# Kernel optimization log

Hardware: AMD Instinct MI355X
Metric: run time of the kernel (lower is better)

Reference implementation:

```python
import jax, jax.numpy as jnp
import numpy as np

B, H, W = 16, 56, 56
CE, CB = 128, 256
NH, WS = 8, 7
HD = CB // NH
N = WS * WS
HID = 4 * CB
EPS = 1e-5


def _rel_pos_index(ws):
    coords = np.stack(np.meshgrid(np.arange(ws), np.arange(ws), indexing='ij')).reshape(2, -1)
    rel = (coords[:, :, None] - coords[:, None, :]).transpose(1, 2, 0).astype(np.int64)
    rel[..., 0] += ws - 1
    rel[..., 1] += ws - 1
    rel[..., 0] *= 2 * ws - 1
    return rel.sum(-1)  # (ws*ws, ws*ws)

RPI = jnp.asarray(_rel_pos_index(WS))


def _ln(x, w, b, axes):
    m = x.mean(axes, keepdims=True)
    v = x.var(axes, keepdims=True)
    return (x - m) * jax.lax.rsqrt(v + EPS) * w + b


def _window_partition(x):  # (B,H,W,C) -> (B*nW, N, C)
    Bx, Hx, Wx, C = x.shape
    x = x.reshape(Bx, Hx // WS, WS, Wx // WS, WS, C)
    return x.transpose(0, 1, 3, 2, 4, 5).reshape(-1, N, C)


def _window_reverse(xw, C):  # (B*nW, N, C) -> (B,H,W,C)
    x = xw.reshape(B, H // WS, W // WS, WS, WS, C)
    return x.transpose(0, 1, 3, 2, 4, 5).reshape(B, H, W, C)


def setup_inputs() -> dict:
    key = jax.random.key(0)
    ks = jax.random.split(key, 12)
    s = 0.02
    return {
        'x_edge': jax.random.normal(ks[0], (B, CE, H, W), jnp.float32),
        'x_body': jax.random.normal(ks[1], (B, H * W, CB), jnp.float32),
        'norm_edge_w': jnp.ones((CE, H, W), jnp.float32),
        'norm_edge_b': jnp.zeros((CE, H, W), jnp.float32),
        'conv_w': jax.random.normal(ks[2], (CB, CE), jnp.float32) * s,
        'norm1_w': jnp.ones((CB,), jnp.float32),
        'norm1_b': jnp.zeros((CB,), jnp.float32),
        'rpb_table': jax.random.normal(ks[3], ((2 * WS - 1) ** 2, NH), jnp.float32) * s,
        'q_w': jax.random.normal(ks[4], (CB, CB), jnp.float32) * s,
        'kv_w': jax.random.normal(ks[5], (2 * CB, CB), jnp.float32) * s,
        'proj_w': jax.random.normal(ks[6], (CB, CB), jnp.float32) * s,
        'proj_b': jnp.zeros((CB,), jnp.float32),
        'norm2_w': jnp.ones((CB,), jnp.float32),
        'norm2_b': jnp.zeros((CB,), jnp.float32),
        'fc1_w': jax.random.normal(ks[7], (HID, CB), jnp.float32) * s,
        'fc1_b': jnp.zeros((HID,), jnp.float32),
        'fc2_w': jax.random.normal(ks[8], (CB, HID), jnp.float32) * s,
        'fc2_b': jnp.zeros((CB,), jnp.float32),
    }


def reference(x_edge, x_body, norm_edge_w, norm_edge_b, conv_w, norm1_w, norm1_b,
              rpb_table, q_w, kv_w, proj_w, proj_b, norm2_w, norm2_b,
              fc1_w, fc1_b, fc2_w, fc2_b):
    x_body_cache = x_body
    scale = HD ** -0.5

    # LayerNorm over (C,H,W) of x_edge, then 1x1 conv (channel mixing), to NHWC
    xe = _ln(x_edge, norm_edge_w, norm_edge_b, axes=(1, 2, 3))  # (B,CE,H,W)
    xe = jnp.einsum('oc,bchw->bhwo', conv_w, xe)                # (B,H,W,CB)

    xb = _ln(x_body, norm1_w, norm1_b, axes=(-1,)).reshape(B, H, W, CB)

    xe_w = _window_partition(xe)  # (Bn,N,CB)
    xb_w = _window_partition(xb)

    q = (xe_w @ q_w.T).reshape(-1, N, NH, HD).transpose(0, 2, 1, 3) * scale  # (Bn,NH,N,HD)
    kv = (xb_w @ kv_w.T).reshape(-1, N, 2, NH, HD).transpose(2, 0, 3, 1, 4)
    k, v = kv[0], kv[1]  # (Bn,NH,N,HD)

    attn = jnp.einsum('bhnd,bhmd->bhnm', q, k)
    bias = rpb_table[RPI.reshape(-1)].reshape(N, N, NH).transpose(2, 0, 1)  # (NH,N,N)
    attn = jax.nn.softmax(attn + bias[None], axis=-1)

    out = jnp.einsum('bhnm,bhmd->bhnd', attn, v).transpose(0, 2, 1, 3).reshape(-1, N, CB)
    out = out @ proj_w.T + proj_b

    x_attn = _window_reverse(out, CB).reshape(B, H * W, CB)
    x = x_body_cache + x_attn

    h = _ln(x, norm2_w, norm2_b, axes=(-1,))
    h = jax.nn.gelu(h @ fc1_w.T + fc1_b, approximate=False) @ fc2_w.T + fc2_b
    x = x + h

    return x.reshape(B, H, W, CB).transpose(0, 3, 1, 2)  # (B,CB,H,W)
```

## Files before the change

### kernel.cpp

```cpp
#include <hip/hip_runtime.h>
#include <hip/hip_bf16.h>
#include <math.h>

#define B_    16
#define CE_   128
#define CB_   256
#define H_    56
#define W_    56
#define NH_   8
#define WS_   7
#define HD_   32
#define NWIN_ 49
#define HW_   3136
#define M_    50176
#define HID_  1024

typedef short bf16x8 __attribute__((ext_vector_type(8)));
typedef float f32x4  __attribute__((ext_vector_type(4)));

__device__ __forceinline__ float waveRedSum(float v) {
#pragma unroll
  for (int off = 32; off; off >>= 1) v += __shfl_xor(v, off, 64);
  return v;
}

__device__ __forceinline__ void load_lds16(const void* g, void* l) {
  __builtin_amdgcn_global_load_lds((__attribute__((address_space(1))) void*)g,
                                   (__attribute__((address_space(3))) void*)l,
                                   16, 0, 0);
}

__global__ void k_stats1(const float* __restrict__ xe, float* __restrict__ part) {
  int blk = blockIdx.x;
  int b = blk >> 6, s = blk & 63;
  const float4* p = (const float4*)(xe + (size_t)b * 401408 + s * 6272);
  float sm = 0.f, s2 = 0.f;
  for (int i = threadIdx.x; i < 1568; i += 256) {
    float4 v = p[i];
    sm += v.x + v.y + v.z + v.w;
    s2 += v.x * v.x + v.y * v.y + v.z * v.z + v.w * v.w;
  }
  sm = waveRedSum(sm); s2 = waveRedSum(s2);
  __shared__ float aux[8];
  int wave = threadIdx.x >> 6, lane = threadIdx.x & 63;
  if (lane == 0) { aux[wave] = sm; aux[4 + wave] = s2; }
  __syncthreads();
  if (threadIdx.x == 0) {
    part[blk * 2]     = aux[0] + aux[1] + aux[2] + aux[3];
    part[blk * 2 + 1] = aux[4] + aux[5] + aux[6] + aux[7];
  }
}

__global__ void k_stats2(const float* __restrict__ part, float* __restrict__ stats) {
  int b = blockIdx.x, lane = threadIdx.x;
  float sm = part[(b * 64 + lane) * 2];
  float s2 = part[(b * 64 + lane) * 2 + 1];
  sm = waveRedSum(sm); s2 = waveRedSum(s2);
  if (lane == 0) {
    float mean = sm / 401408.0f;
    float var  = s2 / 401408.0f - mean * mean;
    stats[b * 2] = mean;
    stats[b * 2 + 1] = rsqrtf(var + 1e-5f);
  }
}

__global__ void k_cast6(const float* __restrict__ s0, const float* __restrict__ s1,
                        const float* __restrict__ s2, const float* __restrict__ s3,
                        const float* __restrict__ s4, const float* __restrict__ s5,
                        __hip_bfloat16* __restrict__ d) {
  size_t i4 = ((size_t)blockIdx.x * 256 + threadIdx.x) * 4;
  if (i4 >= 819200) return;
  const float* src; size_t off;
  if      (i4 < 32768)  { src = s0; off = 0; }
  else if (i4 < 98304)  { src = s1; off = 32768; }
  else if (i4 < 229376) { src = s2; off = 98304; }
  else if (i4 < 294912) { src = s3; off = 229376; }
  else if (i4 < 557056) { src = s4; off = 294912; }
  else                  { src = s5; off = 557056; }
  float4 v = *(const float4*)(src + (i4 - off));
  union { __hip_bfloat16 h[4]; uint2 u; } pk;
  pk.h[0] = __float2bfloat16(v.x);
  pk.h[1] = __float2bfloat16(v.y);
  pk.h[2] = __float2bfloat16(v.z);
  pk.h[3] = __float2bfloat16(v.w);
  *(uint2*)(d + i4) = pk.u;
}

__global__ void k_wqc(const float* __restrict__ qw, const float* __restrict__ cw,
                      __hip_bfloat16* __restrict__ wqc) {
  int o2 = blockIdx.x, c = threadIdx.x;
  float acc = 0.f;
#pragma unroll 4
  for (int o = 0; o < 256; ++o)
    acc += qw[o2 * 256 + o] * cw[o * 128 + c];
  wqc[o2 * 128 + c] = __float2bfloat16(acc * 0.17677669529663687f);
}

__global__ void k_bias_pre(const float* __restrict__ rpb, float* __restrict__ bp) {
  int blk = blockIdx.x;
  int h = blk >> 4, tile = blk & 15;
  int ti = tile >> 2, tj = tile & 3;
  int lane = threadIdx.x;
  int quad = lane >> 4, lm = lane & 15;
  float4 v;
  float* vp = (float*)&v;
#pragma unroll
  for (int r = 0; r < 4; ++r) {
    int i = ti * 16 + quad * 4 + r;
    int j = tj * 16 + lm;
    float b = -1e30f;
    if (i < 49 && j < 49) {
      int rel = (i / 7 - j / 7 + 6) * 13 + (i % 7 - j % 7 + 6);
      b = rpb[rel * 8 + h];
    }
    vp[r] = b;
  }
  *(float4*)&bp[(size_t)(blk * 64 + lane) * 4] = v;
}

__global__ void k_prep_edge(const float* __restrict__ xe,
                            const float* __restrict__ we,
                            const float* __restrict__ be,
                            const float* __restrict__ stats,
                            __hip_bfloat16* __restrict__ Ae) {
  int wb = blockIdx.x;
  int b = wb >> 6, rem = wb & 63;
  int h0 = (rem >> 3) * 7, w0 = (rem & 7) * 7;
  float mean = stats[b * 2], rstd = stats[b * 2 + 1];
  __shared__ __hip_bfloat16 t[49 * 130];
  for (int idx = threadIdx.x; idx < 128 * 49; idx += 256) {
    int c = idx / 49, p = idx % 49;
    int h = h0 + p / 7, w = w0 + p % 7;
    int off = (c * 56 + h) * 56 + w;
    float v = xe[(size_t)b * 401408 + off];
    t[p * 130 + c] = __float2bfloat16((v - mean) * rstd * we[off] + be[off]);
  }
  __syncthreads();
  __hip_bfloat16* dst = Ae + (size_t)wb * 49 * 128;
  for (int idx = threadIdx.x; idx < 49 * 128; idx += 256) {
    int p = idx >> 7, c = idx & 127;
    dst[idx] = t[p * 130 + c];
  }
}

template <bool PERM>
__global__ void k_ln_rows(const float* __restrict__ x,
                          const float* __restrict__ w,
                          const float* __restrict__ bia,
                          __hip_bfloat16* __restrict__ out) {
  int row = blockIdx.x * 4 + (threadIdx.x >> 6);
  int lane = threadIdx.x & 63;
  float4 xv = *(const float4*)(x + (size_t)row * 256 + lane * 4);
  float s  = xv.x + xv.y + xv.z + xv.w;
  float s2 = xv.x * xv.x + xv.y * xv.y + xv.z * xv.z + xv.w * xv.w;
  s = waveRedSum(s); s2 = waveRedSum(s2);
  float mean = s * (1.0f / 256.0f);
  float var  = s2 * (1.0f / 256.0f) - mean * mean;
  float rstd = rsqrtf(var + 1e-5f);
  int orow = row;
  if (PERM) {
    int b = row / 3136, hw = row % 3136;
    int h = hw / 56, ww = hw % 56;
    orow = (b * 64 + (h / 7) * 8 + (ww / 7)) * 49 + (h % 7) * 7 + (ww % 7);
  }
  float4 wv = *(const float4*)(w + lane * 4);
  float4 bv = *(const float4*)(bia + lane * 4);
  union { __hip_bfloat16 h[4]; uint2 u; } pk;
  pk.h[0] = __float2bfloat16((xv.x - mean) * rstd * wv.x + bv.x);
  pk.h[1] = __float2bfloat16((xv.y - mean) * rstd * wv.y + bv.y);
  pk.h[2] = __float2bfloat16((xv.z - mean) * rstd * wv.z + bv.z);
  pk.h[3] = __float2bfloat16((xv.w - mean) * rstd * wv.w + bv.w);
  *(uint2*)(out + (size_t)orow * 256 + lane * 4) = pk.u;
}

template <int EPI, int NX>
__launch_bounds__(256)
__global__ void gemm_bt(const __hip_bfloat16* __restrict__ A,
                        const __hip_bfloat16* __restrict__ Bw,
                        int M, int N, int K,
                        __hip_bfloat16* __restrict__ outb,
                        float* __restrict__ outf,
                        const float* __restrict__ bias,
                        const float* __restrict__ resid) {
  __shared__ __hip_bfloat16 As[4 * 128 * 8];
  __shared__ __hip_bfloat16 Bs[4 * 128 * 8];
  const int tid  = threadIdx.x;
  const int lane = tid & 63;
  const int wave = tid >> 6;
  const int quad = lane >> 4;
  const int lm   = lane & 15;
  const int wm   = (wave & 1) << 6;
  const int wn   = (wave >> 1) << 6;
  const int lin  = blockIdx.x;
  const int slot = lin >> 3;
  const int band = (lin & 7) * 49 + slot / NX;
  const int n0   = (slot % NX) * 128;
  const int m0   = band * 128;

  const int rh = (wave & 1) * 64;
  const int qw = wave >> 1;
  const __hip_bfloat16* Arow = A  + (size_t)(m0 + rh + lane) * K;
  const __hip_bfloat16* Brow = Bw + (size_t)(n0 + rh + lane) * K;

  f32x4 acc[4][4];
#pragma unroll
  for (int i = 0; i < 4; ++i)
#pragma unroll
    for (int j = 0; j < 4; ++j)
#pragma unroll
      for (int r = 0; r < 4; ++r) acc[i][j][r] = 0.f;

  for (int k0 = 0; k0 < K; k0 += 32) {
#pragma unroll
    for (int p = 0; p < 2; ++p) {
      int q = qw + 2 * p;
      load_lds16(Arow + k0 + q * 8, &As[(q * 128 + rh) * 8]);
      load_lds16(Brow + k0 + q * 8, &Bs[(q * 128 + rh) * 8]);
    }
    __syncthreads();
    bf16x8 af[4], bfr[4];
#pragma unroll
    for (int i = 0; i < 4; ++i)
      af[i] = *(const bf16x8*)&As[(quad * 128 + wm + i * 16 + lm) * 8];
#pragma unroll
    for (int j = 0; j < 4; ++j)
      bfr[j] = *(const bf16x8*)&Bs[(quad * 128 + wn + j * 16 + lm) * 8];
#pragma unroll
    for (int i = 0; i < 4; ++i)
#pragma unroll
      for (int j = 0; j < 4; ++j)
        acc[i][j] = __builtin_amdgcn_mfma_f32_16x16x32_bf16(af[i], bfr[j], acc[i][j], 0, 0, 0);
    __syncthreads();
  }

#pragma unroll
  for (int i = 0; i < 4; ++i) {
#pragma unroll
    for (int r = 0; r < 4; ++r) {
      int gm = m0 + wm + i * 16 + quad * 4 + r;
      size_t rowbase;
      if constexpr (EPI == 2) {
        int wb = gm / 49, nn = gm % 49;
        int b = wb >> 6, rem = wb & 63;
        int h = (rem >> 3) * 7 + nn / 7, w = (rem & 7) * 7 + nn % 7;
        rowbase = (size_t)(b * 3136 + h * 56 + w) * 256;
      } else {
        rowbase = (size_t)gm * N;
      }
#pragma unroll
      for (int j = 0; j < 4; ++j) {
        int gn = n0 + wn + j * 16 + lm;
        float v = acc[i][j][r];
        if constexpr (EPI == 0) {
          outb[rowbase + gn] = __float2bfloat16(v);
        } else if constexpr (EPI == 2) {
          outf[rowbase + gn] = v + bias[gn] + resid[rowbase + gn];
        } else if constexpr (EPI == 3) {
          float x = v + bias[gn];
          float y = 0.7978845608028654f * (x + 0.044715f * x * x * x);
          float e = __expf(2.0f * y);
          float th = 1.0f - 2.0f / (e + 1.0f);
          outb[rowbase + gn] = __float2bfloat16(0.5f * x * (1.0f + th));
        } else {
          outf[rowbase + gn] = v + bias[gn] + resid[rowbase + gn];
        }
      }
    }
  }
}

__launch_bounds__(64)
__global__ void k_attn_mfma(const __hip_bfloat16* __restrict__ qb,
                            const __hip_bfloat16* __restrict__ kvb,
                            const float* __restrict__ bp,
                            __hip_bfloat16* __restrict__ ob) {
  int wb = blockIdx.x >> 3;
  int h  = blockIdx.x & 7;
  __shared__ __align__(16) __hip_bfloat16 lds[7424];
  __hip_bfloat16* Qs = lds;
  __hip_bfloat16* Ks = lds + 2560;
  __hip_bfloat16* Vt = lds + 5120;
  __hip_bfloat16* Ps = lds;
  const int lane = threadIdx.x;
  const int quad = lane >> 4, lm = lane & 15;

  const __hip_bfloat16 zb = __float2bfloat16(0.f);
  for (int i = lane; i < 600; i += 64) { Qs[1960 + i] = zb; Ks[1960 + i] = zb; }
  {
    uint4 z; z.x = z.y = z.z = z.w = 0u;
    for (int i = lane; i < 288; i += 64) ((uint4*)Vt)[i] = z;
  }
  {
    int t = lane >> 2, p = lane & 3;
#pragma unroll
    for (int pass = 0; pass < 4; ++pass, t += 16) {
      if (t < 49) {
        size_t rq = (size_t)(wb * 49 + t);
        uint4 qv = *(const uint4*)(qb + rq * 256 + h * 32 + p * 8);
        *(uint4*)&Qs[t * 40 + p * 8] = qv;
        uint4 kv = *(const uint4*)(kvb + rq * 512 + h * 32 + p * 8);
        *(uint4*)&Ks[t * 40 + p * 8] = kv;
        union { uint4 u; __hip_bfloat16 e[8]; } vv;
        vv.u = *(const uint4*)(kvb + rq * 512 + 256 + h * 32 + p * 8);
#pragma unroll
        for (int i = 0; i < 8; ++i) Vt[(p * 8 + i) * 72 + t] = vv.e[i];
      }
    }
  }
  __builtin_amdgcn_s_waitcnt(0);

  bf16x8 qf[4], kf[4];
#pragma unroll
  for (int i = 0; i < 4; ++i) qf[i] = *(const bf16x8*)&Qs[(i * 16 + lm) * 40 + quad * 8];
#pragma unroll
  for (int j = 0; j < 4; ++j) kf[j] = *(const bf16x8*)&Ks[(j * 16 + lm) * 40 + quad * 8];
  f32x4 s[4][4];
#pragma unroll
  for (int i = 0; i < 4; ++i)
#pragma unroll
    for (int j = 0; j < 4; ++j) {
      f32x4 z4; z4[0] = z4[1] = z4[2] = z4[3] = 0.f;
      s[i][j] = __builtin_amdgcn_mfma_f32_16x16x32_bf16(qf[i], kf[j], z4, 0, 0, 0);
    }
#pragma unroll
  for (int ti = 0; ti < 4; ++ti)
#pragma unroll
    for (int tj = 0; tj < 4; ++tj) {
      f32x4 b = *(const f32x4*)&bp[(size_t)(((h * 4 + ti) * 4 + tj) * 64 + lane) * 4];
      s[ti][tj] += b;
    }
  float mrow[4][4], srow[4][4];
#pragma unroll
  for (int ti = 0; ti < 4; ++ti)
#pragma unroll
    for (int r = 0; r < 4; ++r)
      mrow[ti][r] = fmaxf(fmaxf(s[ti][0][r], s[ti][1][r]), fmaxf(s[ti][2][r], s[ti][3][r]));
#pragma unroll
  for (int mask = 1; mask <= 8; mask <<= 1)
#pragma unroll
    for (int ti = 0; ti < 4; ++ti)
#pragma unroll
      for (int r = 0; r < 4; ++r)
        mrow[ti][r] = fmaxf(mrow[ti][r], __shfl_xor(mrow[ti][r], mask, 64));
#pragma unroll
  for (int ti = 0; ti < 4; ++ti)
#pragma unroll
    for (int tj = 0; tj < 4; ++tj)
#pragma unroll
      for (int r = 0; r < 4; ++r)
        s[ti][tj][r] = __expf(s[ti][tj][r] - mrow[ti][r]);
#pragma unroll
  for (int ti = 0; ti < 4; ++ti)
#pragma unroll
    for (int r = 0; r < 4; ++r)
      srow[ti][r] = s[ti][0][r] + s[ti][1][r] + s[ti][2][r] + s[ti][3][r];
#pragma unroll
  for (int mask = 1; mask <= 8; mask <<= 1)
#pragma unroll
    for (int ti = 0; ti < 4; ++ti)
#pragma unroll
      for (int r = 0; r < 4; ++r)
        srow[ti][r] += __shfl_xor(srow[ti][r], mask, 64);
  float inv[4][4];
#pragma unroll
  for (int ti = 0; ti < 4; ++ti)
#pragma unroll
    for (int r = 0; r < 4; ++r)
      inv[ti][r] = 1.0f / srow[ti][r];

#pragma unroll
  for (int ti = 0; ti < 4; ++ti)
#pragma unroll
    for (int tj = 0; tj < 4; ++tj)
#pragma unroll
      for (int r = 0; r < 4; ++r)
        Ps[(ti * 16 + quad * 4 + r) * 72 + tj * 16 + lm] = __float2bfloat16(s[ti][tj][r]);
  __builtin_amdgcn_s_waitcnt(0);

  f32x4 o[4][2];
#pragma unroll
  for (int mt = 0; mt < 4; ++mt)
#pragma unroll
    for (int nt = 0; nt < 2; ++nt)
#pragma unroll
      for (int r = 0; r < 4; ++r) o[mt][nt][r] = 0.f;
#pragma unroll
  for (int kq = 0; kq < 2; ++kq) {
    bf16x8 pa[4], vb[2];
#pragma unroll
    for (int mt = 0; mt < 4; ++mt)
      pa[mt] = *(const bf16x8*)&Ps[(mt * 16 + lm) * 72 + kq * 32 + quad * 8];
#pragma unroll
    for (int nt = 0; nt < 2; ++nt)
      vb[nt] = *(const bf16x8*)&Vt[(nt * 16 + lm) * 72 + kq * 32 + quad * 8];
#pragma unroll
    for (int mt = 0; mt < 4; ++mt)
#pragma unroll
      for (int nt = 0; nt < 2; ++nt)
        o[mt][nt] = __builtin_amdgcn_mfma_f32_16x16x32_bf16(pa[mt], vb[nt], o[mt][nt], 0, 0, 0);
  }
#pragma unroll
  for (int mt = 0; mt < 4; ++mt)
#pragma unroll
    for (int r = 0; r < 4; ++r) {
      int row = mt * 16 + quad * 4 + r;
      if (row < 49) {
#pragma unroll
        for (int nt = 0; nt < 2; ++nt)
          ob[(size_t)(wb * 49 + row) * 256 + h * 32 + nt * 16 + lm] =
              __float2bfloat16(o[mt][nt][r] * inv[mt][r]);
      }
    }
}

__global__ void k_transpose(const float* __restrict__ y, float* __restrict__ out) {
  __shared__ float t[32][33];
  int bb = blockIdx.z;
  int hw0 = blockIdx.x * 32;
  int o0 = blockIdx.y * 32;
  int tx = threadIdx.x, ty = threadIdx.y;
#pragma unroll
  for (int r = 0; r < 4; ++r)
    t[ty + r * 8][tx] = y[(size_t)(bb * 3136 + hw0 + ty + r * 8) * 256 + o0 + tx];
  __syncthreads();
#pragma unroll
  for (int r = 0; r < 4; ++r)
    out[(size_t)(bb * 256 + o0 + ty + r * 8) * 3136 + hw0 + tx] = t[tx][ty + r * 8];
}

extern "C" void kernel_launch(void* const* d_in, const int* in_sizes, int n_in,
                              void* d_out, int out_size, void* d_ws, size_t ws_size,
                              hipStream_t stream) {
  const float* x_edge = (const float*)d_in[0];
  const float* x_body = (const float*)d_in[1];
  const float* ne_w   = (const float*)d_in[2];
  const float* ne_b   = (const float*)d_in[3];
  const float* conv_w = (const float*)d_in[4];
  const float* n1_w   = (const float*)d_in[5];
  const float* n1_b   = (const float*)d_in[6];
  const float* rpb    = (const float*)d_in[7];
  const float* q_w    = (const float*)d_in[8];
  const float* kv_w   = (const float*)d_in[9];
  const float* proj_w = (const float*)d_in[10];
  const float* proj_b = (const float*)d_in[11];
  const float* n2_w   = (const float*)d_in[12];
  const float* n2_b   = (const float*)d_in[13];
  const float* fc1_w  = (const float*)d_in[14];
  const float* fc1_b  = (const float*)d_in[15];
  const float* fc2_w  = (const float*)d_in[16];
  const float* fc2_b  = (const float*)d_in[17];
  float* out = (float*)d_out;
  (void)in_sizes; (void)n_in; (void)out_size; (void)ws_size;

  const size_t SZ_Ae    = (size_t)M_ * 128 * 2;
  const size_t SZ_bf256 = (size_t)M_ * 256 * 2;
  const size_t SZ_bf512 = (size_t)M_ * 512 * 2;
  const size_t SZ_h1    = (size_t)M_ * 1024 * 2;

  char* ws = (char*)d_ws;
  __hip_bfloat16* Wb  = (__hip_bfloat16*)ws;
  float* part  = (float*)(ws + 1638400);
  float* stats = (float*)(ws + 1638400 + 8192);
  float* biasp = (float*)(ws + 1638400 + 8192 + 256);
  __hip_bfloat16* wqc = (__hip_bfloat16*)(ws + 1638400 + 8192 + 256 + 131072);
  char*  P     = ws + 1638400 + 8192 + 256 + 131072 + 65536;
  __hip_bfloat16* w_kv   = Wb + 98304;
  __hip_bfloat16* w_proj = Wb + 229376;
  __hip_bfloat16* w_fc1  = Wb + 294912;
  __hip_bfloat16* w_fc2  = Wb + 557056;
  __hip_bfloat16* Ae    = (__hip_bfloat16*)(P);
  __hip_bfloat16* xbn   = (__hip_bfloat16*)(P + SZ_Ae);
  __hip_bfloat16* qb    = (__hip_bfloat16*)(P + SZ_Ae + SZ_bf256);
  __hip_bfloat16* kvb   = (__hip_bfloat16*)(P + SZ_Ae + 2 * SZ_bf256);
  __hip_bfloat16* attnb = (__hip_bfloat16*)(P + SZ_Ae + 2 * SZ_bf256 + SZ_bf512);
  __hip_bfloat16* h1 = (__hip_bfloat16*)(P);
  char* tail         = P + ((SZ_h1 + 1024 * 1024) & ~(size_t)1023);
  __hip_bfloat16* xn = (__hip_bfloat16*)tail;
  float*          yb = (float*)tail;
  float*          xf = (float*)d_out;

  k_cast6<<<800, 256, 0, stream>>>(conv_w, q_w, kv_w, proj_w, fc1_w, fc2_w, Wb);
  k_wqc<<<256, 128, 0, stream>>>(q_w, conv_w, wqc);
  k_bias_pre<<<128, 64, 0, stream>>>(rpb, biasp);
  k_stats1<<<1024, 256, 0, stream>>>(x_edge, part);
  k_stats2<<<16, 64, 0, stream>>>(part, stats);
  k_prep_edge<<<1024, 256, 0, stream>>>(x_edge, ne_w, ne_b, stats, Ae);
  k_ln_rows<true><<<M_ / 4, 256, 0, stream>>>(x_body, n1_w, n1_b, xbn);
  gemm_bt<0, 2><<<784, 256, 0, stream>>>(Ae, wqc, M_, 256, 128, qb, nullptr, nullptr, nullptr);
  gemm_bt<0, 4><<<1568, 256, 0, stream>>>(xbn, w_kv, M_, 512, 256, kvb, nullptr, nullptr, nullptr);
  k_attn_mfma<<<8192, 64, 0, stream>>>(qb, kvb, biasp, attnb);
  gemm_bt<2, 2><<<784, 256, 0, stream>>>(attnb, w_proj, M_, 256, 256, nullptr, xf, proj_b, x_body);
  k_ln_rows<false><<<M_ / 4, 256, 0, stream>>>(xf, n2_w, n2_b, xn);
  gemm_bt<3, 8><<<3136, 256, 0, stream>>>(xn, w_fc1, M_, 1024, 256, h1, nullptr, fc1_b, nullptr);
  gemm_bt<4, 2><<<784, 256, 0, stream>>>(h1, w_fc2, M_, 256, 1024, nullptr, yb, fc2_b, xf);
  k_transpose<<<dim3(98, 8, 16), dim3(32, 8), 0, stream>>>(yb, out);
}
```

Before: 543.5 us.

## Double-buffer LDS tiles in bf16 GEMM to overlap loads with MFMA

The GEMM kernel now keeps two LDS buffers for the A and B tiles. It issues the direct-to-LDS global loads for the next K-step before running the MFMAs on the current buffer, which replaces the two barriers per iteration with a single vmcnt wait plus barrier. The aim is to hide global-memory latency behind matrix math. In exchange, LDS use doubles and correctness depends on the barrier placed at the end of each iteration before a buffer is reused.

```diff
diff --git a/kernel.cpp b/kernel.cpp
--- a/kernel.cpp
+++ b/kernel.cpp
@@ -182,8 +182,8 @@
                         float* __restrict__ outf,
                         const float* __restrict__ bias,
                         const float* __restrict__ resid) {
-  __shared__ __hip_bfloat16 As[4 * 128 * 8];
-  __shared__ __hip_bfloat16 Bs[4 * 128 * 8];
+  __shared__ __hip_bfloat16 As[2][128 * 32];
+  __shared__ __hip_bfloat16 Bs[2][128 * 32];
   const int tid  = threadIdx.x;
   const int lane = tid & 63;
   const int wave = tid >> 6;
@@ -210,27 +210,42 @@
 #pragma unroll
       for (int r = 0; r < 4; ++r) acc[i][j][r] = 0.f;
 
-  for (int k0 = 0; k0 < K; k0 += 32) {
+  auto STAGE = [&](int buf, int k0) {
 #pragma unroll
     for (int p = 0; p < 2; ++p) {
       int q = qw + 2 * p;
-      load_lds16(Arow + k0 + q * 8, &As[(q * 128 + rh) * 8]);
-      load_lds16(Brow + k0 + q * 8, &Bs[(q * 128 + rh) * 8]);
-    }
-    __syncthreads();
+      load_lds16(Arow + k0 + q * 8, &As[buf][(q * 128 + rh) * 8]);
+      load_lds16(Brow + k0 + q * 8, &Bs[buf][(q * 128 + rh) * 8]);
+    }
+  };
+
+  const int nt = K >> 5;
+  STAGE(0, 0);
+  asm volatile("s_waitcnt vmcnt(0)" ::: "memory");
+  __builtin_amdgcn_s_barrier();
+  __builtin_amdgcn_sched_barrier(0);
+
+  int cur = 0;
+  for (int t = 0; t < nt; ++t) {
+    if (t + 1 < nt) STAGE(cur ^ 1, (t + 1) << 5);
     bf16x8 af[4], bfr[4];
 #pragma unroll
     for (int i = 0; i < 4; ++i)
-      af[i] = *(const bf16x8*)&As[(quad * 128 + wm + i * 16 + lm) * 8];
+      af[i] = *(const bf16x8*)&As[cur][(quad * 128 + wm + i * 16 + lm) * 8];
 #pragma unroll
     for (int j = 0; j < 4; ++j)
-      bfr[j] = *(const bf16x8*)&Bs[(quad * 128 + wn + j * 16 + lm) * 8];
+      bfr[j] = *(const bf16x8*)&Bs[cur][(quad * 128 + wn + j * 16 + lm) * 8];
 #pragma unroll
     for (int i = 0; i < 4; ++i)
 #pragma unroll
       for (int j = 0; j < 4; ++j)
         acc[i][j] = __builtin_amdgcn_mfma_f32_16x16x32_bf16(af[i], bfr[j], acc[i][j], 0, 0, 0);
-    __syncthreads();
+    if (t + 1 < nt) {
+      asm volatile("s_waitcnt vmcnt(0)" ::: "memory");
+      __builtin_amdgcn_s_barrier();
+      __builtin_amdgcn_sched_barrier(0);
+    }
+    cur ^= 1;
   }
 
 #pragma unroll
```

New measurement: 540.7 us. About the same (-0.5%).
